# Kernel optimization log

Hardware: AMD Instinct MI355X
Metric: run time of the kernel (lower is better)

Reference implementation:

```python
import jax, jax.numpy as jnp
import numpy as np

N, K, A = 4096, 64, 8      # nodes, level-2 paths per node, attrs per l2-neighbor
D = 128                    # embed_dim
NU, NR, NA = 100000, 32, 5000  # user vocab, rating vocab, attribute vocab


def setup_inputs() -> dict:
    key = jax.random.key(0)
    ks = jax.random.split(key, 12)
    s = 0.02
    return dict(
        nodes=jax.random.randint(ks[0], (N,), 0, NU),
        paths_rel=jax.random.randint(ks[1], (N, K, 2), 0, NR),
        paths_nbr=jax.random.randint(ks[2], (N, K), 0, NU),
        attrs=jax.random.randint(ks[3], (N, K, A), 0, NA),
        u2e=jax.random.normal(ks[4], (NU, D), dtype=jnp.float32) * s,
        r2e=jax.random.normal(ks[5], (NR, D), dtype=jnp.float32) * s,
        ua2e=jax.random.normal(ks[6], (NA, D), dtype=jnp.float32) * s,
        W1=jax.random.normal(ks[7], (4 * D, 2 * D), dtype=jnp.float32) * s,
        b1=jnp.zeros((2 * D,), jnp.float32),
        W2=jax.random.normal(ks[8], (2 * D, D), dtype=jnp.float32) * s,
        b2=jnp.zeros((D,), jnp.float32),
        A1=jax.random.normal(ks[9], (2 * D, D), dtype=jnp.float32) * s,
        ab1=jnp.zeros((D,), jnp.float32),
        A2=jax.random.normal(ks[10], (D, D), dtype=jnp.float32) * s,
        ab2=jnp.zeros((D,), jnp.float32),
        A3=jax.random.normal(ks[11], (D, 1), dtype=jnp.float32) * s,
        ab3=jnp.zeros((1,), jnp.float32),
    )


def reference(nodes, paths_rel, paths_nbr, attrs, u2e, r2e, ua2e,
              W1, b1, W2, b2, A1, ab1, A2, ab2, A3, ab3):
    # per-path embedding gathers
    r1 = r2e[paths_rel[..., 0]]           # [N,K,D]
    r2 = r2e[paths_rel[..., 1]]           # [N,K,D]
    ne = u2e[paths_nbr]                   # [N,K,D]
    ae = ua2e[attrs].sum(axis=2)          # [N,K,A,D] -> [N,K,D] (uvAttrEmbedding sum)
    # concat + 2-layer MLP (w_r1, w_r2)
    x = jnp.concatenate([r1, r2, ne, ae], axis=-1)   # [N,K,4D]
    h = jax.nn.relu(x @ W1 + b1)                     # [N,K,2D]
    h = jax.nn.relu(h @ W2 + b2)                     # [N,K,D]
    # attention vs self embedding
    self_e = u2e[nodes]                              # [N,D]
    c = jnp.concatenate(
        [h, jnp.broadcast_to(self_e[:, None, :], h.shape)], axis=-1)  # [N,K,2D]
    a = jax.nn.relu(c @ A1 + ab1)
    a = jax.nn.relu(a @ A2 + ab2)
    logits = (a @ A3 + ab3)[..., 0]                  # [N,K]
    w = jax.nn.softmax(logits, axis=1)
    # attention-weighted reduce over paths
    return jnp.einsum('nk,nkd->nd', w, h)            # [N,D]
```

## Files before the change

### kernel.cpp

```cpp
#include <hip/hip_runtime.h>
#include <hip/hip_bf16.h>

#define NN 4096
#define KK 64
#define AA 8
#define DD 128

#define XH_STRIDE 264
#define A_STRIDE  136
#define H2_STRIDE 136
#define XREG_SZ   16896

typedef __bf16 bf16x8 __attribute__((ext_vector_type(8)));
typedef __bf16 bf16x2 __attribute__((ext_vector_type(2)));
typedef float  f32x4  __attribute__((ext_vector_type(4)));

__device__ __forceinline__ short f2bf(float f) {
    unsigned u = __builtin_bit_cast(unsigned, f);
    u += 0x7FFFu + ((u >> 16) & 1u);
    return (short)(u >> 16);
}
__device__ __forceinline__ float bf2f(short s) {
    unsigned u = ((unsigned)(unsigned short)s) << 16;
    return __builtin_bit_cast(float, u);
}
__device__ __forceinline__ unsigned f2bf2(float a, float b) {
#if __has_builtin(__builtin_amdgcn_cvt_pk_bf16_f32)
    bf16x2 r = __builtin_amdgcn_cvt_pk_bf16_f32(a, b);
    return __builtin_bit_cast(unsigned, r);
#else
    return ((unsigned)(unsigned short)f2bf(a)) | (((unsigned)(unsigned short)f2bf(b)) << 16);
#endif
}
__device__ __forceinline__ void store_bf8(short* dst, float4 a, float4 b) {
    uint4 v;
    v.x = f2bf2(a.x, a.y); v.y = f2bf2(a.z, a.w);
    v.z = f2bf2(b.x, b.y); v.w = f2bf2(b.z, b.w);
    *(uint4*)dst = v;
}

__global__ void prep_all(const float* __restrict__ W1, const float* __restrict__ W2,
                         const float* __restrict__ A1, const float* __restrict__ A2,
                         const int* __restrict__ nodes, const float* __restrict__ u2e,
                         const float* __restrict__ ab1,
                         short* __restrict__ W1p, short* __restrict__ W2p,
                         short* __restrict__ A1p, short* __restrict__ A2p,
                         float* __restrict__ s1g)
{
    if (blockIdx.x < 768) {
        int t = blockIdx.x * 256 + threadIdx.x;
        const float* src; short* dst; int Ncols, ksl, idx;
        if (t < 131072)      { src = W1; dst = W1p; Ncols = 256; ksl = 4; idx = t; }
        else if (t < 163840) { src = W2; dst = W2p; Ncols = 128; ksl = 3; idx = t - 131072; }
        else if (t < 180224) { src = A1; dst = A1p; Ncols = 128; ksl = 2; idx = t - 163840; }
        else                 { src = A2; dst = A2p; Ncols = 128; ksl = 2; idx = t - 180224; }
        int j     = idx & 7;
        int lane  = (idx >> 3) & 63;
        int fi    = idx >> 9;
        int kstep = fi & ((1 << ksl) - 1);
        int ntile = fi >> ksl;
        int k  = kstep * 32 + (lane >> 4) * 8 + j;
        int nn = ntile * 16 + (lane & 15);
        dst[idx] = f2bf(src[(size_t)k * Ncols + nn]);
    } else {
        __shared__ float rows[8][DD];
        const int b = blockIdx.x - 768;
        {
            const int r  = threadIdx.x >> 5;
            const int c4 = (threadIdx.x & 31) * 4;
            const int node = nodes[b * 8 + r];
            *(float4*)&rows[r][c4] = *(const float4*)&u2e[(size_t)node * DD + c4];
        }
        __syncthreads();
        const int h = threadIdx.x >> 7;
        const int c = threadIdx.x & 127;
        const float ab = ab1[c];
        float acc[4] = {ab, ab, ab, ab};
        for (int i = 0; i < DD; ++i) {
            const float av = A1[(size_t)(DD + i) * DD + c];
#pragma unroll
            for (int j = 0; j < 4; ++j)
                acc[j] = fmaf(rows[h * 4 + j][i], av, acc[j]);
        }
#pragma unroll
        for (int j = 0; j < 4; ++j)
            s1g[(size_t)(b * 8 + h * 4 + j) * DD + c] = acc[j];
    }
}

__launch_bounds__(512, 4)
__global__ void l2agg_mfma(
    const int* __restrict__ paths_rel,
    const int* __restrict__ paths_nbr,
    const int* __restrict__ attrs,
    const float* __restrict__ u2e,
    const float* __restrict__ r2e,
    const float* __restrict__ ua2e,
    const float* __restrict__ b1,
    const float* __restrict__ b2,
    const float* __restrict__ ab2,
    const float* __restrict__ A3,
    const float* __restrict__ ab3,
    const short* __restrict__ W1p,
    const short* __restrict__ W2p,
    const short* __restrict__ A1p,
    const short* __restrict__ A2p,
    const float* __restrict__ s1g,
    float* __restrict__ out)
{
    __shared__ short xa[XREG_SZ];
    __shared__ short xb[XREG_SZ];
    __shared__ int   idx_u[576];
    __shared__ float wts8[512];
    float* partials = (float*)idx_u;

    const int n    = blockIdx.x;
    const int tid  = threadIdx.x;
    const int lane = tid & 63;
    const int wv   = tid >> 6;
    const int mr   = lane & 15;
    const int q    = lane >> 4;

    {
        const int* ab = attrs + (size_t)n * KK * AA;
        __builtin_amdgcn_global_load_lds(
            (const __attribute__((address_space(1))) void*)(ab + wv * 64 + lane),
            (__attribute__((address_space(3))) void*)(idx_u + wv * 64), 4, 0, 0);
        if (wv == 0) {
            const int* nb = paths_nbr + (size_t)n * KK;
            __builtin_amdgcn_global_load_lds(
                (const __attribute__((address_space(1))) void*)(nb + lane),
                (__attribute__((address_space(3))) void*)(idx_u + 512), 4, 0, 0);
        }
    }

#pragma unroll
    for (int pass = 0; pass < 2; ++pass) {
        const int p  = pass * 32 + (tid >> 4);
        const int t  = tid & 15;
        const int o  = t * 8;
        const int pk = n * KK + p;
        const int i0 = paths_rel[pk * 2 + 0];
        const int i1 = paths_rel[pk * 2 + 1];
        float4 r1a = *(const float4*)&r2e[(size_t)i0 * DD + o];
        float4 r1b = *(const float4*)&r2e[(size_t)i0 * DD + o + 4];
        float4 r2a = *(const float4*)&r2e[(size_t)i1 * DD + o];
        float4 r2b = *(const float4*)&r2e[(size_t)i1 * DD + o + 4];
        store_bf8(&xa[p * XH_STRIDE + o], r1a, r1b);
        store_bf8(&xa[p * XH_STRIDE + 128 + o], r2a, r2b);
    }
    __syncthreads();

    const short* W1b = W1p + wv * 2 * 16 * 512 + lane * 8;
    f32x4 acc1[4][2] = {};
    bf16x8 bfc[2], bfn[2];
#pragma unroll
    for (int nt = 0; nt < 2; ++nt) bfc[nt] = *(const bf16x8*)&W1b[nt * 8192];
#pragma unroll
    for (int ks = 0; ks < 8; ++ks) {
#pragma unroll
        for (int nt = 0; nt < 2; ++nt)
            bfn[nt] = *(const bf16x8*)&W1b[nt * 8192 + (ks + 1) * 512];
        bf16x8 af[4];
#pragma unroll
        for (int mt = 0; mt < 4; ++mt)
            af[mt] = *(const bf16x8*)&xa[(mt * 16 + mr) * XH_STRIDE + ks * 32 + q * 8];
#pragma unroll
        for (int nt = 0; nt < 2; ++nt)
#pragma unroll
            for (int mt = 0; mt < 4; ++mt)
                acc1[mt][nt] = __builtin_amdgcn_mfma_f32_16x16x32_bf16(af[mt], bfc[nt], acc1[mt][nt], 0, 0, 0);
#pragma unroll
        for (int nt = 0; nt < 2; ++nt) bfc[nt] = bfn[nt];
    }

    __builtin_amdgcn_sched_barrier(0);

#pragma unroll
    for (int pass = 0; pass < 2; ++pass) {
        const int p  = pass * 32 + (tid >> 4);
        const int t  = tid & 15;
        const int o  = t * 8;
        const int nb = idx_u[512 + p];
        float4 nea = *(const float4*)&u2e[(size_t)nb * DD + o];
        float4 neb = *(const float4*)&u2e[(size_t)nb * DD + o + 4];
        float4 aea = make_float4(0.f, 0.f, 0.f, 0.f);
        float4 aeb = make_float4(0.f, 0.f, 0.f, 0.f);
#pragma unroll
        for (int a = 0; a < AA; ++a) {
            const int ai = idx_u[p * AA + a];
            float4 va = *(const float4*)&ua2e[(size_t)ai * DD + o];
            float4 vb = *(const float4*)&ua2e[(size_t)ai * DD + o + 4];
            aea.x += va.x; aea.y += va.y; aea.z += va.z; aea.w += va.w;
            aeb.x += vb.x; aeb.y += vb.y; aeb.z += vb.z; aeb.w += vb.w;
        }
        store_bf8(&xb[p * XH_STRIDE + o], nea, neb);
        store_bf8(&xb[p * XH_STRIDE + 128 + o], aea, aeb);
    }
    __builtin_amdgcn_sched_barrier(0);
    __syncthreads();

#pragma unroll
    for (int ks = 8; ks < 16; ++ks) {
        if (ks < 15) {
#pragma unroll
            for (int nt = 0; nt < 2; ++nt)
                bfn[nt] = *(const bf16x8*)&W1b[nt * 8192 + (ks + 1) * 512];
        }
        bf16x8 af[4];
#pragma unroll
        for (int mt = 0; mt < 4; ++mt)
            af[mt] = *(const bf16x8*)&xb[(mt * 16 + mr) * XH_STRIDE + (ks - 8) * 32 + q * 8];
#pragma unroll
        for (int nt = 0; nt < 2; ++nt)
#pragma unroll
            for (int mt = 0; mt < 4; ++mt)
                acc1[mt][nt] = __builtin_amdgcn_mfma_f32_16x16x32_bf16(af[mt], bfc[nt], acc1[mt][nt], 0, 0, 0);
        if (ks < 15) {
#pragma unroll
            for (int nt = 0; nt < 2; ++nt) bfc[nt] = bfn[nt];
        }
    }

    const short* W2b = W2p + wv * 8 * 512 + lane * 8;
    bf16x8 g2c = *(const bf16x8*)&W2b[0], g2n;

#pragma unroll
    for (int nt = 0; nt < 2; ++nt) {
        const int col = (wv * 2 + nt) * 16 + mr;
        const float bb = b1[col];
#pragma unroll
        for (int mt = 0; mt < 4; ++mt)
#pragma unroll
            for (int r = 0; r < 4; r += 2) {
                unsigned pk2 = f2bf2(fmaxf(acc1[mt][nt][r] + bb, 0.f),
                                     fmaxf(acc1[mt][nt][r + 1] + bb, 0.f));
                xa[(mt * 16 + q * 4 + r)     * XH_STRIDE + col] = (short)pk2;
                xa[(mt * 16 + q * 4 + r + 1) * XH_STRIDE + col] = (short)(pk2 >> 16);
            }
    }
    __syncthreads();

    f32x4 acc2[4] = {};
#pragma unroll
    for (int ks = 0; ks < 8; ++ks) {
        if (ks < 7) g2n = *(const bf16x8*)&W2b[(ks + 1) * 512];
        bf16x8 af[4];
#pragma unroll
        for (int mt = 0; mt < 4; ++mt)
            af[mt] = *(const bf16x8*)&xa[(mt * 16 + mr) * XH_STRIDE + ks * 32 + q * 8];
#pragma unroll
        for (int mt = 0; mt < 4; ++mt)
            acc2[mt] = __builtin_amdgcn_mfma_f32_16x16x32_bf16(af[mt], g2c, acc2[mt], 0, 0, 0);
        if (ks < 7) g2c = g2n;
    }

    const short* A1b = A1p + wv * 4 * 512 + lane * 8;
    bf16x8 g3f[4];
#pragma unroll
    for (int ks = 0; ks < 4; ++ks) g3f[ks] = *(const bf16x8*)&A1b[ks * 512];
    const float s1v = s1g[(size_t)n * DD + wv * 16 + mr];

    {
        const int col = wv * 16 + mr;
        const float bb = b2[col];
#pragma unroll
        for (int mt = 0; mt < 4; ++mt)
#pragma unroll
            for (int r = 0; r < 4; r += 2) {
                unsigned pk2 = f2bf2(fmaxf(acc2[mt][r] + bb, 0.f),
                                     fmaxf(acc2[mt][r + 1] + bb, 0.f));
                xb[(mt * 16 + q * 4 + r)     * H2_STRIDE + col] = (short)pk2;
                xb[(mt * 16 + q * 4 + r + 1) * H2_STRIDE + col] = (short)(pk2 >> 16);
            }
    }
    __syncthreads();

    {
        f32x4 acc3[4];
#pragma unroll
        for (int mt = 0; mt < 4; ++mt) {
            acc3[mt][0] = s1v; acc3[mt][1] = s1v; acc3[mt][2] = s1v; acc3[mt][3] = s1v;
        }
#pragma unroll
        for (int ks = 0; ks < 4; ++ks) {
            bf16x8 af[4];
#pragma unroll
            for (int mt = 0; mt < 4; ++mt)
                af[mt] = *(const bf16x8*)&xb[(mt * 16 + mr) * H2_STRIDE + ks * 32 + q * 8];
#pragma unroll
            for (int mt = 0; mt < 4; ++mt)
                acc3[mt] = __builtin_amdgcn_mfma_f32_16x16x32_bf16(af[mt], g3f[ks], acc3[mt], 0, 0, 0);
        }
        const short* A2b = A2p + wv * 4 * 512 + lane * 8;
        bf16x8 g4f[4];
#pragma unroll
        for (int ks = 0; ks < 4; ++ks) g4f[ks] = *(const bf16x8*)&A2b[ks * 512];

        {
            const int col = wv * 16 + mr;
#pragma unroll
            for (int mt = 0; mt < 4; ++mt)
#pragma unroll
                for (int r = 0; r < 4; r += 2) {
                    unsigned pk2 = f2bf2(fmaxf(acc3[mt][r], 0.f),
                                         fmaxf(acc3[mt][r + 1], 0.f));
                    xa[(mt * 16 + q * 4 + r)     * A_STRIDE + col] = (short)pk2;
                    xa[(mt * 16 + q * 4 + r + 1) * A_STRIDE + col] = (short)(pk2 >> 16);
                }
        }
        __syncthreads();

        f32x4 acc4[4];
        {
            const float bv = ab2[wv * 16 + mr];
#pragma unroll
            for (int mt = 0; mt < 4; ++mt) {
                acc4[mt][0] = bv; acc4[mt][1] = bv; acc4[mt][2] = bv; acc4[mt][3] = bv;
            }
        }
#pragma unroll
        for (int ks = 0; ks < 4; ++ks) {
            bf16x8 af[4];
#pragma unroll
            for (int mt = 0; mt < 4; ++mt)
                af[mt] = *(const bf16x8*)&xa[(mt * 16 + mr) * A_STRIDE + ks * 32 + q * 8];
#pragma unroll
            for (int mt = 0; mt < 4; ++mt)
                acc4[mt] = __builtin_amdgcn_mfma_f32_16x16x32_bf16(af[mt], g4f[ks], acc4[mt], 0, 0, 0);
        }
        const float av = A3[wv * 16 + mr];
        float pl[4][4];
#pragma unroll
        for (int mt = 0; mt < 4; ++mt)
#pragma unroll
            for (int r = 0; r < 4; ++r)
                pl[mt][r] = fmaxf(acc4[mt][r], 0.f) * av;
#pragma unroll
        for (int off = 1; off < 16; off <<= 1)
#pragma unroll
            for (int mt = 0; mt < 4; ++mt)
#pragma unroll
                for (int r = 0; r < 4; ++r)
                    pl[mt][r] += __shfl_xor(pl[mt][r], off, 64);
        if (mr == 0) {
#pragma unroll
            for (int mt = 0; mt < 4; ++mt)
#pragma unroll
                for (int r = 0; r < 4; ++r)
                    partials[wv * KK + mt * 16 + q * 4 + r] = pl[mt][r];
        }
    }
    __syncthreads();

    {
        float l = ab3[0];
#pragma unroll
        for (int w = 0; w < 8; ++w) l += partials[w * KK + lane];
        float m = l;
#pragma unroll
        for (int off = 32; off > 0; off >>= 1) m = fmaxf(m, __shfl_xor(m, off, 64));
        float e = expf(l - m);
        float s = e;
#pragma unroll
        for (int off = 32; off > 0; off >>= 1) s += __shfl_xor(s, off, 64);
        wts8[wv * 64 + lane] = e / s;
        const int col = wv * 16 + mr;
        const float* wl = &wts8[wv * 64 + q * 16];
        const short* hp = &xb[(q * 16) * H2_STRIDE + col];
        float acc = 0.f;
#pragma unroll
        for (int j = 0; j < 16; ++j)
            acc = fmaf(wl[j], bf2f(hp[j * H2_STRIDE]), acc);
        acc += __shfl_xor(acc, 16, 64);
        acc += __shfl_xor(acc, 32, 64);
        if (q == 0) out[(size_t)n * DD + col] = acc;
    }
}

extern "C" void kernel_launch(void* const* d_in, const int* in_sizes, int n_in,
                              void* d_out, int out_size, void* d_ws, size_t ws_size,
                              hipStream_t stream)
{
    const int*   nodes     = (const int*)d_in[0];
    const int*   paths_rel = (const int*)d_in[1];
    const int*   paths_nbr = (const int*)d_in[2];
    const int*   attrs     = (const int*)d_in[3];
    const float* u2e  = (const float*)d_in[4];
    const float* r2e  = (const float*)d_in[5];
    const float* ua2e = (const float*)d_in[6];
    const float* W1   = (const float*)d_in[7];
    const float* b1   = (const float*)d_in[8];
    const float* W2   = (const float*)d_in[9];
    const float* b2   = (const float*)d_in[10];
    const float* A1   = (const float*)d_in[11];
    const float* ab1  = (const float*)d_in[12];
    const float* A2   = (const float*)d_in[13];
    const float* ab2  = (const float*)d_in[14];
    const float* A3   = (const float*)d_in[15];
    const float* ab3  = (const float*)d_in[16];
    float* out = (float*)d_out;

    short* wsp = (short*)d_ws;
    short* W1p = wsp;
    short* W2p = wsp + 131072;
    short* A1p = wsp + 163840;
    short* A2p = wsp + 180224;
    float* s1g = (float*)((char*)d_ws + 393216);

    hipLaunchKernelGGL(prep_all, dim3(768 + 512), dim3(256), 0, stream,
                       W1, W2, A1, A2, nodes, u2e, ab1,
                       W1p, W2p, A1p, A2p, s1g);
    hipLaunchKernelGGL(l2agg_mfma, dim3(NN), dim3(512), 0, stream,
                       paths_rel, paths_nbr, attrs, u2e, r2e, ua2e,
                       b1, b2, ab2, A3, ab3,
                       W1p, W2p, A1p, A2p, s1g, out);
}
```

Measured before the change: 287.8 us.

## Split GEMM work across waves in a 2x4 M-by-N grid

Result: slower. 308.8 us (+7.3%).

```diff
diff --git a/kernel.cpp b/kernel.cpp
--- a/kernel.cpp
+++ b/kernel.cpp
@@ -120,6 +120,8 @@
     const int wv   = tid >> 6;
     const int mr   = lane & 15;
     const int q    = lane >> 4;
+    const int wm   = wv >> 2;
+    const int wn   = wv & 3;
 
     {
         const int* ab = attrs + (size_t)n * KK * AA;
@@ -151,27 +153,27 @@
     }
     __syncthreads();
 
-    const short* W1b = W1p + wv * 2 * 16 * 512 + lane * 8;
-    f32x4 acc1[4][2] = {};
-    bf16x8 bfc[2], bfn[2];
-#pragma unroll
-    for (int nt = 0; nt < 2; ++nt) bfc[nt] = *(const bf16x8*)&W1b[nt * 8192];
+    const short* W1b = W1p + wn * 4 * 8192 + lane * 8;
+    f32x4 acc1[2][4] = {};
+    bf16x8 bfc[4], bfn[4];
+#pragma unroll
+    for (int nt = 0; nt < 4; ++nt) bfc[nt] = *(const bf16x8*)&W1b[nt * 8192];
 #pragma unroll
     for (int ks = 0; ks < 8; ++ks) {
 #pragma unroll
-        for (int nt = 0; nt < 2; ++nt)
+        for (int nt = 0; nt < 4; ++nt)
             bfn[nt] = *(const bf16x8*)&W1b[nt * 8192 + (ks + 1) * 512];
-        bf16x8 af[4];
-#pragma unroll
-        for (int mt = 0; mt < 4; ++mt)
-            af[mt] = *(const bf16x8*)&xa[(mt * 16 + mr) * XH_STRIDE + ks * 32 + q * 8];
-#pragma unroll
-        for (int nt = 0; nt < 2; ++nt)
-#pragma unroll
-            for (int mt = 0; mt < 4; ++mt)
+        bf16x8 af[2];
+#pragma unroll
+        for (int mt = 0; mt < 2; ++mt)
+            af[mt] = *(const bf16x8*)&xa[(wm * 32 + mt * 16 + mr) * XH_STRIDE + ks * 32 + q * 8];
+#pragma unroll
+        for (int nt = 0; nt < 4; ++nt)
+#pragma unroll
+            for (int mt = 0; mt < 2; ++mt)
                 acc1[mt][nt] = __builtin_amdgcn_mfma_f32_16x16x32_bf16(af[mt], bfc[nt], acc1[mt][nt], 0, 0, 0);
 #pragma unroll
-        for (int nt = 0; nt < 2; ++nt) bfc[nt] = bfn[nt];
+        for (int nt = 0; nt < 4; ++nt) bfc[nt] = bfn[nt];
     }
 
     __builtin_amdgcn_sched_barrier(0);
@@ -204,151 +206,183 @@
     for (int ks = 8; ks < 16; ++ks) {
         if (ks < 15) {
 #pragma unroll
-            for (int nt = 0; nt < 2; ++nt)
+            for (int nt = 0; nt < 4; ++nt)
                 bfn[nt] = *(const bf16x8*)&W1b[nt * 8192 + (ks + 1) * 512];
         }
-        bf16x8 af[4];
-#pragma unroll
-        for (int mt = 0; mt < 4; ++mt)
-            af[mt] = *(const bf16x8*)&xb[(mt * 16 + mr) * XH_STRIDE + (ks - 8) * 32 + q * 8];
-#pragma unroll
-        for (int nt = 0; nt < 2; ++nt)
-#pragma unroll
-            for (int mt = 0; mt < 4; ++mt)
+        bf16x8 af[2];
+#pragma unroll
+        for (int mt = 0; mt < 2; ++mt)
+            af[mt] = *(const bf16x8*)&xb[(wm * 32 + mt * 16 + mr) * XH_STRIDE + (ks - 8) * 32 + q * 8];
+#pragma unroll
+        for (int nt = 0; nt < 4; ++nt)
+#pragma unroll
+            for (int mt = 0; mt < 2; ++mt)
                 acc1[mt][nt] = __builtin_amdgcn_mfma_f32_16x16x32_bf16(af[mt], bfc[nt], acc1[mt][nt], 0, 0, 0);
         if (ks < 15) {
 #pragma unroll
-            for (int nt = 0; nt < 2; ++nt) bfc[nt] = bfn[nt];
-        }
-    }
-
-    const short* W2b = W2p + wv * 8 * 512 + lane * 8;
-    bf16x8 g2c = *(const bf16x8*)&W2b[0], g2n;
-
-#pragma unroll
-    for (int nt = 0; nt < 2; ++nt) {
-        const int col = (wv * 2 + nt) * 16 + mr;
+            for (int nt = 0; nt < 4; ++nt) bfc[nt] = bfn[nt];
+        }
+    }
+
+    const short* W2b = W2p + wn * 2 * 4096 + lane * 8;
+    bf16x8 g2c[2], g2n[2];
+#pragma unroll
+    for (int nt = 0; nt < 2; ++nt) g2c[nt] = *(const bf16x8*)&W2b[nt * 4096];
+
+#pragma unroll
+    for (int nt = 0; nt < 4; ++nt) {
+        const int col = (wn * 4 + nt) * 16 + mr;
         const float bb = b1[col];
 #pragma unroll
-        for (int mt = 0; mt < 4; ++mt)
+        for (int mt = 0; mt < 2; ++mt)
 #pragma unroll
             for (int r = 0; r < 4; r += 2) {
                 unsigned pk2 = f2bf2(fmaxf(acc1[mt][nt][r] + bb, 0.f),
                                      fmaxf(acc1[mt][nt][r + 1] + bb, 0.f));
-                xa[(mt * 16 + q * 4 + r)     * XH_STRIDE + col] = (short)pk2;
-                xa[(mt * 16 + q * 4 + r + 1) * XH_STRIDE + col] = (short)(pk2 >> 16);
+                xa[(wm * 32 + mt * 16 + q * 4 + r)     * XH_STRIDE + col] = (short)pk2;
+                xa[(wm * 32 + mt * 16 + q * 4 + r + 1) * XH_STRIDE + col] = (short)(pk2 >> 16);
             }
     }
     __syncthreads();
 
-    f32x4 acc2[4] = {};
+    f32x4 acc2[2][2] = {};
 #pragma unroll
     for (int ks = 0; ks < 8; ++ks) {
-        if (ks < 7) g2n = *(const bf16x8*)&W2b[(ks + 1) * 512];
-        bf16x8 af[4];
-#pragma unroll
-        for (int mt = 0; mt < 4; ++mt)
-            af[mt] = *(const bf16x8*)&xa[(mt * 16 + mr) * XH_STRIDE + ks * 32 + q * 8];
-#pragma unroll
-        for (int mt = 0; mt < 4; ++mt)
-            acc2[mt] = __builtin_amdgcn_mfma_f32_16x16x32_bf16(af[mt], g2c, acc2[mt], 0, 0, 0);
-        if (ks < 7) g2c = g2n;
-    }
-
-    const short* A1b = A1p + wv * 4 * 512 + lane * 8;
-    bf16x8 g3f[4];
-#pragma unroll
-    for (int ks = 0; ks < 4; ++ks) g3f[ks] = *(const bf16x8*)&A1b[ks * 512];
-    const float s1v = s1g[(size_t)n * DD + wv * 16 + mr];
+        if (ks < 7) {
+#pragma unroll
+            for (int nt = 0; nt < 2; ++nt)
+                g2n[nt] = *(const bf16x8*)&W2b[nt * 4096 + (ks + 1) * 512];
+        }
+        bf16x8 af[2];
+#pragma unroll
+        for (int mt = 0; mt < 2; ++mt)
+            af[mt] = *(const bf16x8*)&xa[(wm * 32 + mt * 16 + mr) * XH_STRIDE + ks * 32 + q * 8];
+#pragma unroll
+        for (int nt = 0; nt < 2; ++nt)
+#pragma unroll
+            for (int mt = 0; mt < 2; ++mt)
+                acc2[mt][nt] = __builtin_amdgcn_mfma_f32_16x16x32_bf16(af[mt], g2c[nt], acc2[mt][nt], 0, 0, 0);
+        if (ks < 7) {
+#pragma unroll
+            for (int nt = 0; nt < 2; ++nt) g2c[nt] = g2n[nt];
+        }
+    }
+
+    const short* A1b = A1p + wn * 2 * 2048 + lane * 8;
+    bf16x8 g3f[2][4];
+#pragma unroll
+    for (int nt = 0; nt < 2; ++nt)
+#pragma unroll
+        for (int ks = 0; ks < 4; ++ks) g3f[nt][ks] = *(const bf16x8*)&A1b[nt * 2048 + ks * 512];
+    float s1v[2];
+#pragma unroll
+    for (int nt = 0; nt < 2; ++nt)
+        s1v[nt] = s1g[(size_t)n * DD + (wn * 2 + nt) * 16 + mr];
+
+#pragma unroll
+    for (int nt = 0; nt < 2; ++nt) {
+        const int col = (wn * 2 + nt) * 16 + mr;
+        const float bb = b2[col];
+#pragma unroll
+        for (int mt = 0; mt < 2; ++mt)
+#pragma unroll
+            for (int r = 0; r < 4; r += 2) {
+                unsigned pk2 = f2bf2(fmaxf(acc2[mt][nt][r] + bb, 0.f),
+                                     fmaxf(acc2[mt][nt][r + 1] + bb, 0.f));
+                xb[(wm * 32 + mt * 16 + q * 4 + r)     * H2_STRIDE + col] = (short)pk2;
+                xb[(wm * 32 + mt * 16 + q * 4 + r + 1) * H2_STRIDE + col] = (short)(pk2 >> 16);
+            }
+    }
+    __syncthreads();
 
     {
-        const int col = wv * 16 + mr;
-        const float bb = b2[col];
-#pragma unroll
-        for (int mt = 0; mt < 4; ++mt)
-#pragma unroll
-            for (int r = 0; r < 4; r += 2) {
-                unsigned pk2 = f2bf2(fmaxf(acc2[mt][r] + bb, 0.f),
-                                     fmaxf(acc2[mt][r + 1] + bb, 0.f));
-                xb[(mt * 16 + q * 4 + r)     * H2_STRIDE + col] = (short)pk2;
-                xb[(mt * 16 + q * 4 + r + 1) * H2_STRIDE + col] = (short)(pk2 >> 16);
+        f32x4 acc3[2][2];
+#pragma unroll
+        for (int mt = 0; mt < 2; ++mt)
+#pragma unroll
+            for (int nt = 0; nt < 2; ++nt) {
+                acc3[mt][nt][0] = s1v[nt]; acc3[mt][nt][1] = s1v[nt];
+                acc3[mt][nt][2] = s1v[nt]; acc3[mt][nt][3] = s1v[nt];
             }
-    }
-    __syncthreads();
-
-    {
-        f32x4 acc3[4];
-#pragma unroll
-        for (int mt = 0; mt < 4; ++mt) {
-            acc3[mt][0] = s1v; acc3[mt][1] = s1v; acc3[mt][2] = s1v; acc3[mt][3] = s1v;
-        }
 #pragma unroll
         for (int ks = 0; ks < 4; ++ks) {
-            bf16x8 af[4];
-#pragma unroll
-            for (int mt = 0; mt < 4; ++mt)
-                af[mt] = *(const bf16x8*)&xb[(mt * 16 + mr) * H2_STRIDE + ks * 32 + q * 8];
-#pragma unroll
-            for (int mt = 0; mt < 4; ++mt)
-                acc3[mt] = __builtin_amdgcn_mfma_f32_16x16x32_bf16(af[mt], g3f[ks], acc3[mt], 0, 0, 0);
-        }
-        const short* A2b = A2p + wv * 4 * 512 + lane * 8;
-        bf16x8 g4f[4];
-#pragma unroll
-        for (int ks = 0; ks < 4; ++ks) g4f[ks] = *(const bf16x8*)&A2b[ks * 512];
-
-        {
-            const int col = wv * 16 + mr;
-#pragma unroll
-            for (int mt = 0; mt < 4; ++mt)
+            bf16x8 af[2];
+#pragma unroll
+            for (int mt = 0; mt < 2; ++mt)
+                af[mt] = *(const bf16x8*)&xb[(wm * 32 + mt * 16 + mr) * H2_STRIDE + ks * 32 + q * 8];
+#pragma unroll
+            for (int nt = 0; nt < 2; ++nt)
+#pragma unroll
+                for (int mt = 0; mt < 2; ++mt)
+                    acc3[mt][nt] = __builtin_amdgcn_mfma_f32_16x16x32_bf16(af[mt], g3f[nt][ks], acc3[mt][nt], 0, 0, 0);
+        }
+        const short* A2b = A2p + wn * 2 * 2048 + lane * 8;
+        bf16x8 g4f[2][4];
+#pragma unroll
+        for (int nt = 0; nt < 2; ++nt)
+#pragma unroll
+            for (int ks = 0; ks < 4; ++ks) g4f[nt][ks] = *(const bf16x8*)&A2b[nt * 2048 + ks * 512];
+
+#pragma unroll
+        for (int nt = 0; nt < 2; ++nt) {
+            const int col = (wn * 2 + nt) * 16 + mr;
+#pragma unroll
+            for (int mt = 0; mt < 2; ++mt)
 #pragma unroll
                 for (int r = 0; r < 4; r += 2) {
-                    unsigned pk2 = f2bf2(fmaxf(acc3[mt][r], 0.f),
-                                         fmaxf(acc3[mt][r + 1], 0.f));
-                    xa[(mt * 16 + q * 4 + r)     * A_STRIDE + col] = (short)pk2;
-                    xa[(mt * 16 + q * 4 + r + 1) * A_STRIDE + col] = (short)(pk2 >> 16);
+                    unsigned pk2 = f2bf2(fmaxf(acc3[mt][nt][r], 0.f),
+                                         fmaxf(acc3[mt][nt][r + 1], 0.f));
+                    xa[(wm * 32 + mt * 16 + q * 4 + r)     * A_STRIDE + col] = (short)pk2;
+                    xa[(wm * 32 + mt * 16 + q * 4 + r + 1) * A_STRIDE + col] = (short)(pk2 >> 16);
                 }
         }
         __syncthreads();
 
-        f32x4 acc4[4];
-        {
-            const float bv = ab2[wv * 16 + mr];
-#pragma unroll
-            for (int mt = 0; mt < 4; ++mt) {
-                acc4[mt][0] = bv; acc4[mt][1] = bv; acc4[mt][2] = bv; acc4[mt][3] = bv;
+        f32x4 acc4[2][2];
+#pragma unroll
+        for (int nt = 0; nt < 2; ++nt) {
+            const float bv = ab2[(wn * 2 + nt) * 16 + mr];
+#pragma unroll
+            for (int mt = 0; mt < 2; ++mt) {
+                acc4[mt][nt][0] = bv; acc4[mt][nt][1] = bv;
+                acc4[mt][nt][2] = bv; acc4[mt][nt][3] = bv;
             }
         }
 #pragma unroll
         for (int ks = 0; ks < 4; ++ks) {
-            bf16x8 af[4];
-#pragma unroll
-            for (int mt = 0; mt < 4; ++mt)
-                af[mt] = *(const bf16x8*)&xa[(mt * 16 + mr) * A_STRIDE + ks * 32 + q * 8];
-#pragma unroll
-            for (int mt = 0; mt < 4; ++mt)
-                acc4[mt] = __builtin_amdgcn_mfma_f32_16x16x32_bf16(af[mt], g4f[ks], acc4[mt], 0, 0, 0);
-        }
-        const float av = A3[wv * 16 + mr];
-        float pl[4][4];
-#pragma unroll
-        for (int mt = 0; mt < 4; ++mt)
+            bf16x8 af[2];
+#pragma unroll
+            for (int mt = 0; mt < 2; ++mt)
+                af[mt] = *(const bf16x8*)&xa[(wm * 32 + mt * 16 + mr) * A_STRIDE + ks * 32 + q * 8];
+#pragma unroll
+            for (int nt = 0; nt < 2; ++nt)
+#pragma unroll
+                for (int mt = 0; mt < 2; ++mt)
+                    acc4[mt][nt] = __builtin_amdgcn_mfma_f32_16x16x32_bf16(af[mt], g4f[nt][ks], acc4[mt][nt], 0, 0, 0);
+        }
+        float av[2];
+#pragma unroll
+        for (int nt = 0; nt < 2; ++nt) av[nt] = A3[(wn * 2 + nt) * 16 + mr];
+        float pl[2][4];
+#pragma unroll
+        for (int mt = 0; mt < 2; ++mt)
 #pragma unroll
             for (int r = 0; r < 4; ++r)
-                pl[mt][r] = fmaxf(acc4[mt][r], 0.f) * av;
+                pl[mt][r] = fmaxf(acc4[mt][0][r], 0.f) * av[0]
+                          + fmaxf(acc4[mt][1][r], 0.f) * av[1];
 #pragma unroll
         for (int off = 1; off < 16; off <<= 1)
 #pragma unroll
-            for (int mt = 0; mt < 4; ++mt)
+            for (int mt = 0; mt < 2; ++mt)
 #pragma unroll
                 for (int r = 0; r < 4; ++r)
                     pl[mt][r] += __shfl_xor(pl[mt][r], off, 64);
         if (mr == 0) {
 #pragma unroll
-            for (int mt = 0; mt < 4; ++mt)
+            for (int mt = 0; mt < 2; ++mt)
 #pragma unroll
                 for (int r = 0; r < 4; ++r)
-                    partials[wv * KK + mt * 16 + q * 4 + r] = pl[mt][r];
+                    partials[wn * 64 + wm * 32 + mt * 16 + q * 4 + r] = pl[mt][r];
         }
     }
     __syncthreads();
@@ -356,7 +390,7 @@
     {
         float l = ab3[0];
 #pragma unroll
-        for (int w = 0; w < 8; ++w) l += partials[w * KK + lane];
+        for (int w = 0; w < 4; ++w) l += partials[w * 64 + lane];
         float m = l;
 #pragma unroll
         for (int off = 32; off > 0; off >>= 1) m = fmaxf(m, __shfl_xor(m, off, 64));
```
